# Kernel optimization log

Hardware: AMD Instinct MI355X
Metric: run time of the kernel (lower is better)

The kernel has to match this reference:

```python
import jax, jax.numpy as jnp
import numpy as np

LOSS_WEIGHT = 1.0
INTENSITY_WEIGHT = 0.5


def setup_inputs() -> dict:
    key = jax.random.key(0)
    k1, k2 = jax.random.split(key)
    N, M = 20000, 20000
    adv_pc = jax.random.normal(k1, (N, 4), dtype=jnp.float32)
    ori_pc = jax.random.normal(k2, (M, 4), dtype=jnp.float32)
    return {"adv_pc": adv_pc, "ori_pc": ori_pc}


def reference(adv_pc, ori_pc):
    adv_xyz = adv_pc[:, :3]  # [N,3]
    ori_xyz = ori_pc[:, :3]  # [M,3]

    # Squared pairwise distances via |a|^2 + |b|^2 - 2 a.b  -> [N,M]
    a2 = jnp.sum(adv_xyz * adv_xyz, axis=1)  # [N]
    b2 = jnp.sum(ori_xyz * ori_xyz, axis=1)  # [M]
    d2 = a2[:, None] + b2[None, :] - 2.0 * (adv_xyz @ ori_xyz.T)

    # 1-NN in both directions (knn_points with K=1 returns squared dists)
    min_dist_adv_to_ori = jnp.min(d2, axis=1)     # [N]
    adv_indices = jnp.argmin(d2, axis=1)          # [N] nearest ori for each adv
    min_dist_ori_to_adv = jnp.min(d2, axis=0)     # [M]
    ori_indices = jnp.argmin(d2, axis=0)          # [M] nearest adv for each ori

    chamfer_loss = jnp.mean(min_dist_adv_to_ori) + jnp.mean(min_dist_ori_to_adv)

    adv_intensity = adv_pc[:, 3]
    ori_intensity = ori_pc[:, 3]
    adv_intensity_diff_1 = jnp.mean((adv_intensity - ori_intensity[adv_indices]) ** 2)
    adv_intensity_diff_2 = jnp.mean((ori_intensity - adv_intensity[ori_indices]) ** 2)
    intensity_loss = (adv_intensity_diff_1 + adv_intensity_diff_2) / 2.0

    return chamfer_loss * LOSS_WEIGHT + intensity_loss * INTENSITY_WEIGHT
```

## Files before the change

kernel.cpp:

```cpp
#include <hip/hip_runtime.h>

#define CH 512
#define TPCH 16
#define QPB 128
#define YSL 8
#define RB 64

typedef __bf16 bf16x8 __attribute__((ext_vector_type(8)));
typedef float f32x16 __attribute__((ext_vector_type(16)));

__device__ __forceinline__ unsigned bfb(float x) {
    __bf16 h = (__bf16)x;
    return (unsigned)__builtin_bit_cast(unsigned short, h);
}
__device__ __forceinline__ float bff(unsigned b) {
    return (float)__builtin_bit_cast(__bf16, (unsigned short)b);
}

__global__ __launch_bounds__(256) void init_keys(unsigned long long* keys, int n) {
    int i = blockIdx.x * blockDim.x + threadIdx.x;
    if (i < n) keys[i] = 0xFFFFFFFFFFFFFFFFull;
}

__device__ __forceinline__ void stage_one(uint4* a_lds, int local, float4 p, bool valid) {
    float x, y, z, u;
    if (valid) {
        x = p.x; y = p.y; z = p.z;
        u = 0.25f * fmaf(p.x, p.x, fmaf(p.y, p.y, p.z * p.z));
    } else {
        x = 0.f; y = 0.f; z = 0.f; u = 130.f;
    }
    unsigned xh = bfb(x); unsigned xl = bfb(x - bff(xh));
    unsigned yh = bfb(y); unsigned yl = bfb(y - bff(yh));
    unsigned zh = bfb(z); unsigned zl = bfb(z - bff(zh));
    unsigned uh = bfb(u); float u1 = u - bff(uh);
    unsigned ul = bfb(u1); unsigned ull = bfb(u1 - bff(ul));
    uint4 h0, h1;
    h0.x = xh | (xl << 16); h0.y = h0.x;
    h0.z = yh | (yl << 16); h0.w = h0.z;
    h1.x = zh | (zl << 16); h1.y = h1.x;
    h1.z = uh | (ul << 16);
    h1.w = ull | (0x43A0u << 16);
    int t = local >> 5, r = local & 31;
    a_lds[t * 64 + r]      = h0;
    a_lds[t * 64 + 32 + r] = h1;
}

__global__ __launch_bounds__(256, 4) void mfma_nn(
    const float4* __restrict__ adv, int N,
    const float4* __restrict__ ori, int M,
    unsigned long long* __restrict__ keys0,
    unsigned long long* __restrict__ keys1,
    int chunks)
{
    const int dir = blockIdx.z;
    const float4* __restrict__ q = dir ? ori : adv;
    const float4* __restrict__ t = dir ? adv : ori;
    const int nq = dir ? M : N;
    const int nt = dir ? N : M;
    unsigned long long* __restrict__ out = dir ? keys1 : keys0;

    const int tid = threadIdx.x;
    const int wave = tid >> 6;
    const int lane = tid & 63;
    const int col = lane & 31;
    const int h = lane >> 5;

    const int qi = blockIdx.x * QPB + wave * 32 + col;
    const bool qv = qi < nq;
    float4 qp = qv ? q[qi] : make_float4(0.f, 0.f, 0.f, 0.f);

    float cx = -0.5f * qp.x, cy = -0.5f * qp.y, cz = -0.5f * qp.z;
    unsigned cxh = bfb(cx); unsigned cxl = bfb(cx - bff(cxh));
    unsigned cyh = bfb(cy); unsigned cyl = bfb(cy - bff(cyh));
    unsigned czh = bfb(cz); unsigned czl = bfb(cz - bff(czh));
    uint4 braw;
    if (h == 0) {
        braw.x = cxh | (cxh << 16); braw.y = cxl | (cxl << 16);
        braw.z = cyh | (cyh << 16); braw.w = cyl | (cyl << 16);
    } else {
        braw.x = czh | (czh << 16); braw.y = czl | (czl << 16);
        braw.z = 0x3F803F80u;       braw.w = 0x3F803F80u;
    }
    const bf16x8 bfrag = __builtin_bit_cast(bf16x8, braw);

    __shared__ uint4 a_lds[TPCH * 64];
    const f32x16 zero = {};

    const int slicebase = blockIdx.y * chunks * CH;
    unsigned cm = 0xFFFFFFFFu;
    int base = slicebase;

    int j0 = base + tid, j1 = base + tid + 256;
    bool v0 = j0 < nt, v1 = j1 < nt;
    float4 pf0 = v0 ? t[j0] : make_float4(0.f, 0.f, 0.f, 0.f);
    float4 pf1 = v1 ? t[j1] : make_float4(0.f, 0.f, 0.f, 0.f);

    for (int c = 0; c < chunks; ++c) {
        if (c) __syncthreads();
        stage_one(a_lds, tid,       pf0, v0);
        stage_one(a_lds, tid + 256, pf1, v1);
        __syncthreads();

        const int nb = base + CH;
        if (c + 1 < chunks) {
            j0 = nb + tid; j1 = nb + tid + 256;
            v0 = j0 < nt;  v1 = j1 < nt;
            pf0 = v0 ? t[j0] : make_float4(0.f, 0.f, 0.f, 0.f);
            pf1 = v1 ? t[j1] : make_float4(0.f, 0.f, 0.f, 0.f);
        }

        const unsigned tl0 = (unsigned)(c << 4);
        #pragma unroll
        for (int tt = 0; tt < TPCH; ++tt) {
            bf16x8 a = __builtin_bit_cast(bf16x8, a_lds[tt * 64 + lane]);
            f32x16 acc = __builtin_amdgcn_mfma_f32_32x32x16_bf16(a, bfrag, zero, 0, 0, 0);

            unsigned u0 = min(min(__float_as_uint(acc[0]),  __float_as_uint(acc[1])),  __float_as_uint(acc[2]));
            unsigned u1 = min(min(__float_as_uint(acc[3]),  __float_as_uint(acc[4])),  __float_as_uint(acc[5]));
            unsigned u2 = min(min(__float_as_uint(acc[6]),  __float_as_uint(acc[7])),  __float_as_uint(acc[8]));
            unsigned u3 = min(min(__float_as_uint(acc[9]),  __float_as_uint(acc[10])), __float_as_uint(acc[11]));
            unsigned u4 = min(min(__float_as_uint(acc[12]), __float_as_uint(acc[13])), __float_as_uint(acc[14]));
            unsigned u5 = min(min(u0, u1), u2);
            unsigned u6 = min(min(u3, u4), __float_as_uint(acc[15]));
            unsigned m  = min(u5, u6);

            cm = min(cm, (m << 9) | (tl0 + (unsigned)tt));
        }
        base = nb;
    }

    const int jb = slicebase + (int)(cm & 0x7Fu) * 32 + 4 * h;
    unsigned long long run = 0xFFFFFFFFFFFFFFFFull;
    #pragma unroll
    for (int e = 0; e < 16; ++e) {
        int r = (e & 3) + ((e >> 2) << 3);
        int j = jb + r;
        if (j < nt) {
            float4 b = t[j];
            float dx = qp.x - b.x, dy = qp.y - b.y, dz = qp.z - b.z;
            float d2 = fmaf(dx, dx, fmaf(dy, dy, dz * dz));
            unsigned long long cand =
                ((unsigned long long)__float_as_uint(d2) << 32) | (unsigned)j;
            run = cand < run ? cand : run;
        }
    }

    unsigned long long other = __shfl_xor(run, 32);
    run = run < other ? run : other;
    if (h == 0 && qv) {
        unsigned jw = (unsigned)(run & 0xFFFFFFFFu);
        if (jw < (unsigned)nt) atomicMin(out + qi, run);
    }
}

__device__ inline float block_reduce_sum(float v, float* lds) {
    #pragma unroll
    for (int off = 32; off > 0; off >>= 1) v += __shfl_down(v, off, 64);
    int wave = threadIdx.x >> 6;
    int lane = threadIdx.x & 63;
    __syncthreads();
    if (lane == 0) lds[wave] = v;
    __syncthreads();
    float r = 0.f;
    if (threadIdx.x == 0) {
        #pragma unroll
        for (int w = 0; w < 4; ++w) r += lds[w];
    }
    return r;
}

__global__ __launch_bounds__(256) void partial_finalize(
    const unsigned long long* __restrict__ keys0, int n,
    const unsigned long long* __restrict__ keys1, int m,
    const float4* __restrict__ adv, const float4* __restrict__ ori,
    float* __restrict__ partials)
{
    __shared__ float lds[4];
    float s_min0 = 0.f, s_i1 = 0.f, s_min1 = 0.f, s_i2 = 0.f;
    const int stride = RB * 256;
    const int t0 = blockIdx.x * 256 + threadIdx.x;

    for (int i = t0; i < n; i += stride) {
        int j = (int)(unsigned int)(keys0[i] & 0xFFFFFFFFu);
        float4 a = adv[i];
        float4 b = ori[j];
        float dx = a.x - b.x, dy = a.y - b.y, dz = a.z - b.z;
        s_min0 += fmaf(dx, dx, fmaf(dy, dy, dz * dz));
        float dw = a.w - b.w;
        s_i1 += dw * dw;
    }
    for (int j = t0; j < m; j += stride) {
        int i = (int)(unsigned int)(keys1[j] & 0xFFFFFFFFu);
        float4 b = ori[j];
        float4 a = adv[i];
        float dx = b.x - a.x, dy = b.y - a.y, dz = b.z - a.z;
        s_min1 += fmaf(dx, dx, fmaf(dy, dy, dz * dz));
        float dw = b.w - a.w;
        s_i2 += dw * dw;
    }

    float r0 = block_reduce_sum(s_min0, lds);
    float r1 = block_reduce_sum(s_i1, lds);
    float r2 = block_reduce_sum(s_min1, lds);
    float r3 = block_reduce_sum(s_i2, lds);

    if (threadIdx.x == 0) {
        partials[blockIdx.x * 4 + 0] = r0;
        partials[blockIdx.x * 4 + 1] = r1;
        partials[blockIdx.x * 4 + 2] = r2;
        partials[blockIdx.x * 4 + 3] = r3;
    }
}

__global__ __launch_bounds__(256) void combine(
    const float* __restrict__ partials, int n, int m, float* __restrict__ out)
{
    __shared__ float lds[4];
    float v0 = 0.f, v1 = 0.f, v2 = 0.f, v3 = 0.f;
    if (threadIdx.x < RB) {
        v0 = partials[threadIdx.x * 4 + 0];
        v1 = partials[threadIdx.x * 4 + 1];
        v2 = partials[threadIdx.x * 4 + 2];
        v3 = partials[threadIdx.x * 4 + 3];
    }
    float r0 = block_reduce_sum(v0, lds);
    float r1 = block_reduce_sum(v1, lds);
    float r2 = block_reduce_sum(v2, lds);
    float r3 = block_reduce_sum(v3, lds);
    if (threadIdx.x == 0) {
        float chamfer   = r0 / (float)n + r2 / (float)m;
        float intensity = 0.5f * (r1 / (float)n + r3 / (float)m);
        out[0] = chamfer * 1.0f + intensity * 0.5f;
    }
}

extern "C" void kernel_launch(void* const* d_in, const int* in_sizes, int n_in,
                              void* d_out, int out_size, void* d_ws, size_t ws_size,
                              hipStream_t stream) {
    const float4* adv = (const float4*)d_in[0];
    const float4* ori = (const float4*)d_in[1];
    const int N = in_sizes[0] / 4;
    const int M = in_sizes[1] / 4;

    unsigned long long* keys0 = (unsigned long long*)d_ws;
    unsigned long long* keys1 = keys0 + N;
    float* partials = (float*)(keys1 + M);
    float* out = (float*)d_out;

    init_keys<<<(N + M + 255) / 256, 256, 0, stream>>>(keys0, N + M);

    const int ntmax = max(N, M);
    const int chunks = (ntmax + YSL * CH - 1) / (YSL * CH);
    const int qmax = max(N, M);
    dim3 grid((qmax + QPB - 1) / QPB, YSL, 2);
    mfma_nn<<<grid, 256, 0, stream>>>(adv, N, ori, M, keys0, keys1, chunks);

    partial_finalize<<<RB, 256, 0, stream>>>(keys0, N, keys1, M, adv, ori, partials);
    combine<<<1, 256, 0, stream>>>(partials, N, M, out);
}
```

Before: 52.53 us.

## Replace atomicMin keys with per-slice slots and drop init kernel

Result: faster. 49.33 us (-6.1%).

```diff
diff --git a/kernel.cpp b/kernel.cpp
--- a/kernel.cpp
+++ b/kernel.cpp
@@ -15,11 +15,6 @@
 }
 __device__ __forceinline__ float bff(unsigned b) {
     return (float)__builtin_bit_cast(__bf16, (unsigned short)b);
-}
-
-__global__ __launch_bounds__(256) void init_keys(unsigned long long* keys, int n) {
-    int i = blockIdx.x * blockDim.x + threadIdx.x;
-    if (i < n) keys[i] = 0xFFFFFFFFFFFFFFFFull;
 }
 
 __device__ __forceinline__ void stage_one(uint4* a_lds, int local, float4 p, bool valid) {
@@ -46,11 +41,10 @@
     a_lds[t * 64 + 32 + r] = h1;
 }
 
-__global__ __launch_bounds__(256, 4) void mfma_nn(
+__global__ __launch_bounds__(256, 6) void mfma_nn(
     const float4* __restrict__ adv, int N,
     const float4* __restrict__ ori, int M,
-    unsigned long long* __restrict__ keys0,
-    unsigned long long* __restrict__ keys1,
+    unsigned long long* __restrict__ slots, int S,
     int chunks)
 {
     const int dir = blockIdx.z;
@@ -58,7 +52,8 @@
     const float4* __restrict__ t = dir ? adv : ori;
     const int nq = dir ? M : N;
     const int nt = dir ? N : M;
-    unsigned long long* __restrict__ out = dir ? keys1 : keys0;
+    unsigned long long* __restrict__ outrow =
+        slots + (size_t)(dir * YSL + blockIdx.y) * (size_t)S;
 
     const int tid = threadIdx.x;
     const int wave = tid >> 6;
@@ -91,10 +86,17 @@
     unsigned cm = 0xFFFFFFFFu;
     int base = slicebase;
 
-    int j0 = base + tid, j1 = base + tid + 256;
-    bool v0 = j0 < nt, v1 = j1 < nt;
-    float4 pf0 = v0 ? t[j0] : make_float4(0.f, 0.f, 0.f, 0.f);
-    float4 pf1 = v1 ? t[j1] : make_float4(0.f, 0.f, 0.f, 0.f);
+    float4 pf0, pf1; bool v0, v1;
+    {
+        int j0 = base + tid, j1 = j0 + 256;
+        if (base + CH <= nt) {
+            pf0 = t[j0]; pf1 = t[j1]; v0 = true; v1 = true;
+        } else {
+            v0 = j0 < nt; v1 = j1 < nt;
+            pf0 = v0 ? t[j0] : make_float4(0.f, 0.f, 0.f, 0.f);
+            pf1 = v1 ? t[j1] : make_float4(0.f, 0.f, 0.f, 0.f);
+        }
+    }
 
     for (int c = 0; c < chunks; ++c) {
         if (c) __syncthreads();
@@ -104,10 +106,14 @@
 
         const int nb = base + CH;
         if (c + 1 < chunks) {
-            j0 = nb + tid; j1 = nb + tid + 256;
-            v0 = j0 < nt;  v1 = j1 < nt;
-            pf0 = v0 ? t[j0] : make_float4(0.f, 0.f, 0.f, 0.f);
-            pf1 = v1 ? t[j1] : make_float4(0.f, 0.f, 0.f, 0.f);
+            int j0 = nb + tid, j1 = j0 + 256;
+            if (nb + CH <= nt) {
+                pf0 = t[j0]; pf1 = t[j1]; v0 = true; v1 = true;
+            } else {
+                v0 = j0 < nt; v1 = j1 < nt;
+                pf0 = v0 ? t[j0] : make_float4(0.f, 0.f, 0.f, 0.f);
+                pf1 = v1 ? t[j1] : make_float4(0.f, 0.f, 0.f, 0.f);
+            }
         }
 
         const unsigned tl0 = (unsigned)(c << 4);
@@ -148,10 +154,7 @@
 
     unsigned long long other = __shfl_xor(run, 32);
     run = run < other ? run : other;
-    if (h == 0 && qv) {
-        unsigned jw = (unsigned)(run & 0xFFFFFFFFu);
-        if (jw < (unsigned)nt) atomicMin(out + qi, run);
-    }
+    if (h == 0 && qv) outrow[qi] = run;
 }
 
 __device__ inline float block_reduce_sum(float v, float* lds) {
@@ -171,8 +174,8 @@
 }
 
 __global__ __launch_bounds__(256) void partial_finalize(
-    const unsigned long long* __restrict__ keys0, int n,
-    const unsigned long long* __restrict__ keys1, int m,
+    const unsigned long long* __restrict__ slots, int S,
+    int n, int m,
     const float4* __restrict__ adv, const float4* __restrict__ ori,
     float* __restrict__ partials)
 {
@@ -180,23 +183,25 @@
     float s_min0 = 0.f, s_i1 = 0.f, s_min1 = 0.f, s_i2 = 0.f;
     const int stride = RB * 256;
     const int t0 = blockIdx.x * 256 + threadIdx.x;
+    const unsigned long long* __restrict__ s0 = slots;
+    const unsigned long long* __restrict__ s1 = slots + (size_t)YSL * S;
 
     for (int i = t0; i < n; i += stride) {
-        int j = (int)(unsigned int)(keys0[i] & 0xFFFFFFFFu);
-        float4 a = adv[i];
-        float4 b = ori[j];
-        float dx = a.x - b.x, dy = a.y - b.y, dz = a.z - b.z;
-        s_min0 += fmaf(dx, dx, fmaf(dy, dy, dz * dz));
-        float dw = a.w - b.w;
+        unsigned long long k = s0[i];
+        #pragma unroll
+        for (int y = 1; y < YSL; ++y) k = min(k, s0[(size_t)y * S + i]);
+        int j = (int)(unsigned int)(k & 0xFFFFFFFFu);
+        s_min0 += __uint_as_float((unsigned int)(k >> 32));
+        float dw = adv[i].w - ori[j].w;
         s_i1 += dw * dw;
     }
-    for (int j = t0; j < m; j += stride) {
-        int i = (int)(unsigned int)(keys1[j] & 0xFFFFFFFFu);
-        float4 b = ori[j];
-        float4 a = adv[i];
-        float dx = b.x - a.x, dy = b.y - a.y, dz = b.z - a.z;
-        s_min1 += fmaf(dx, dx, fmaf(dy, dy, dz * dz));
-        float dw = b.w - a.w;
+    for (int jj = t0; jj < m; jj += stride) {
+        unsigned long long k = s1[jj];
+        #pragma unroll
+        for (int y = 1; y < YSL; ++y) k = min(k, s1[(size_t)y * S + jj]);
+        int i = (int)(unsigned int)(k & 0xFFFFFFFFu);
+        s_min1 += __uint_as_float((unsigned int)(k >> 32));
+        float dw = ori[jj].w - adv[i].w;
         s_i2 += dw * dw;
     }
 
@@ -242,20 +247,16 @@
     const float4* ori = (const float4*)d_in[1];
     const int N = in_sizes[0] / 4;
     const int M = in_sizes[1] / 4;
-
-    unsigned long long* keys0 = (unsigned long long*)d_ws;
-    unsigned long long* keys1 = keys0 + N;
-    float* partials = (float*)(keys1 + M);
+    const int S = max(N, M);
+
+    unsigned long long* slots = (unsigned long long*)d_ws;
+    float* partials = (float*)(slots + (size_t)2 * YSL * S);
     float* out = (float*)d_out;
 
-    init_keys<<<(N + M + 255) / 256, 256, 0, stream>>>(keys0, N + M);
-
-    const int ntmax = max(N, M);
-    const int chunks = (ntmax + YSL * CH - 1) / (YSL * CH);
-    const int qmax = max(N, M);
-    dim3 grid((qmax + QPB - 1) / QPB, YSL, 2);
-    mfma_nn<<<grid, 256, 0, stream>>>(adv, N, ori, M, keys0, keys1, chunks);
-
-    partial_finalize<<<RB, 256, 0, stream>>>(keys0, N, keys1, M, adv, ori, partials);
+    const int chunks = (S + YSL * CH - 1) / (YSL * CH);
+    dim3 grid((S + QPB - 1) / QPB, YSL, 2);
+    mfma_nn<<<grid, 256, 0, stream>>>(adv, N, ori, M, slots, S, chunks);
+
+    partial_finalize<<<RB, 256, 0, stream>>>(slots, S, N, M, adv, ori, partials);
     combine<<<1, 256, 0, stream>>>(partials, N, M, out);
 }
```
